# Kernel optimization log

Measured on AMD Instinct MI355X. Metric: run time of the kernel, lower is better.

## Reference

```python
import jax, jax.numpy as jnp
import numpy as np

NUM_HEADS = 16


def setup_inputs() -> dict:
    rng = jax.random.key(0)
    ks = jax.random.split(rng, 11)
    T, B, E = 1024, 4, 1024
    s = E ** -0.5  # weight init scale
    return {
        "query": jax.random.normal(ks[0], (T, B, E), jnp.float32),
        "key": jax.random.normal(ks[1], (T, B, E), jnp.float32),
        "value": jax.random.normal(ks[2], (T, B, E), jnp.float32),
        "q_proj_weight": jax.random.normal(ks[3], (E, E), jnp.float32) * s,
        "k_proj_weight1": jax.random.normal(ks[4], (E, E), jnp.float32) * s,
        "k_proj_weight2": jax.random.normal(ks[5], (E, E), jnp.float32) * s,
        "v_proj_weight": jax.random.normal(ks[6], (E, E), jnp.float32) * s,
        "in_proj_bias": jax.random.normal(ks[7], (4 * E,), jnp.float32) * 0.02,
        "out_proj_weight": jax.random.normal(ks[8], (E, E), jnp.float32) * s,
        "out_proj_bias": jax.random.normal(ks[9], (E,), jnp.float32) * 0.02,
        "pi": jax.random.uniform(ks[10], (2, NUM_HEADS), jnp.float32, 0.3, 0.7),
    }


def reference(query, key, value, q_proj_weight, k_proj_weight1, k_proj_weight2,
              v_proj_weight, in_proj_bias, out_proj_weight, out_proj_bias, pi):
    T, Bz, E = query.shape
    H = NUM_HEADS
    hd = E // H
    scaling = hd ** -0.5

    b_q, b_k1, b_k2, b_v = jnp.split(in_proj_bias, 4)
    q = query @ q_proj_weight.T + b_q
    k1 = key @ k_proj_weight1.T + b_k1
    k2 = key @ k_proj_weight2.T + b_k2
    v = value @ v_proj_weight.T + b_v

    def heads(x):  # (S, B, E) -> (B*H, S, hd)
        S = x.shape[0]
        return x.reshape(S, Bz * H, hd).transpose(1, 0, 2)

    q, k1, k2, v = heads(q), heads(k1), heads(k2), heads(v)

    def sqdist(a, b):  # (B*H, Nt, hd), (B*H, Ns, hd) -> (B*H, Nt, Ns)
        a2 = jnp.sum(a * a, axis=-1)
        b2 = jnp.sum(b * b, axis=-1)
        ab = jnp.einsum('btd,bsd->bts', a, b)
        return a2[:, :, None] + b2[:, None, :] - 2.0 * ab

    e1 = jnp.exp(-scaling / 2.0 * sqdist(q, k1))
    e2 = jnp.exp(-3.0 * scaling / 2.0 * sqdist(q, k2))

    pi1 = jnp.clip(jnp.abs(pi[0]), 1e-6, 2.0)  # (H,)
    pi2 = jnp.clip(jnp.abs(pi[1]), 1e-6, 2.0)

    Nt, Ns = e1.shape[1], e1.shape[2]
    attn = (e1.reshape(Bz, H, Nt, Ns) * pi1[None, :, None, None]
            + e2.reshape(Bz, H, Nt, Ns) * pi2[None, :, None, None])
    attn = attn.reshape(Bz * H, Nt, Ns)
    attn = attn / (jnp.sum(attn, axis=-1, keepdims=True) + 1e-6)

    out = jnp.einsum('bts,bsd->btd', attn, v)        # (B*H, Nt, hd)
    out = out.transpose(1, 0, 2).reshape(T, Bz, E)   # (T, B, E)
    return out @ out_proj_weight.T + out_proj_bias
```

## Files before the change

### kernel.cpp

```cpp
#include <hip/hip_runtime.h>
#include <hip/hip_bf16.h>

#define T_DIM 1024
#define B_DIM 4
#define E_DIM 1024
#define H_DIM 16
#define HD    64
#define M_DIM (T_DIM * B_DIM)

typedef __hip_bfloat16 bf16;
typedef __bf16 bf16x8 __attribute__((ext_vector_type(8)));
typedef __bf16 bf16x4 __attribute__((ext_vector_type(4)));
typedef float  f32x4  __attribute__((ext_vector_type(4)));

#define P4S ((size_t)M_DIM * E_DIM)
#define P1S ((size_t)E_DIM * E_DIM)

__global__ __launch_bounds__(256) void cvt_all(
    const float* __restrict__ q, const float* __restrict__ k,
    const float* __restrict__ v, const float* __restrict__ w0,
    const float* __restrict__ w1, const float* __restrict__ w2,
    const float* __restrict__ w3, const float* __restrict__ w4,
    __bf16* __restrict__ dst)
{
  size_t i = ((size_t)blockIdx.x * 256 + threadIdx.x) * 8;
  const float* src;
  size_t off;
  if (i < P4S)            { src = q; off = i; }
  else if (i < 2 * P4S)   { src = k; off = i - P4S; }
  else if (i < 3 * P4S)   { src = v; off = i - 2 * P4S; }
  else {
    size_t j = i - 3 * P4S;
    int wsel = (int)(j >> 20);
    off = j & (P1S - 1);
    const float* ws[5] = {w0, w1, w2, w3, w4};
    src = ws[wsel];
  }
  float4 a = *(const float4*)(src + off);
  float4 b = *(const float4*)(src + off + 4);
  bf16x8 o;
  o[0] = (__bf16)a.x; o[1] = (__bf16)a.y; o[2] = (__bf16)a.z; o[3] = (__bf16)a.w;
  o[4] = (__bf16)b.x; o[5] = (__bf16)b.y; o[6] = (__bf16)b.z; o[7] = (__bf16)b.w;
  *(bf16x8*)(dst + i) = o;
}

__device__ __forceinline__ void load_lds16(const __bf16* g, __bf16* l) {
  __builtin_amdgcn_global_load_lds(
      (__attribute__((address_space(1))) void*)(void*)g,
      (__attribute__((address_space(3))) void*)l, 16, 0, 0);
}
__device__ __forceinline__ void load_lds4(const float* g, float* l) {
  __builtin_amdgcn_global_load_lds(
      (__attribute__((address_space(1))) void*)(void*)g,
      (__attribute__((address_space(3))) void*)l, 4, 0, 0);
}

__device__ __forceinline__ void stage_half(
    int H, const __bf16* __restrict__ X, const __bf16* __restrict__ W,
    int bm, int bn, __bf16* As, __bf16* Bs, int tid)
{
  if (H >= 64) return;
  const int T  = H >> 2;
  const int h  = H & 3;
  const int rh = (h & 1) * 128;
  const __bf16* src = (h < 2) ? X : W;
  const int rbase   = (h < 2) ? bm : bn;
  __bf16* lb = ((h < 2) ? As : Bs) + (T & 1) * 16384;
#pragma unroll
  for (int li = 0; li < 2; ++li) {
    int r  = rh + li * 64 + (tid >> 3);
    int gc = (tid & 7) ^ (r & 7);
    load_lds16(src + (size_t)(rbase + r) * E_DIM + T * 64 + gc * 8,
               lb + (rh + li * 64) * 64 + tid * 8);
  }
}

#define RD(base, row, c) \
  (*(const bf16x8*)((base) + (row) * 64 + ((((c) ^ ((row) & 7))) << 3)))

__global__ __launch_bounds__(512, 2) void proj_gemm4(
    const __bf16* __restrict__ xbase, const __bf16* __restrict__ wbase,
    const float* __restrict__ bin, __bf16* __restrict__ cbase)
{
  __shared__ __bf16 lds[65536];
  __bf16* As = lds;
  __bf16* Bs = lds + 32768;

  const int z = blockIdx.z;
  const __bf16* X = xbase + ((z == 0) ? 0 : (z == 3) ? 2 * P4S : P4S);
  const __bf16* W = wbase + (size_t)z * P1S;
  const float* bias = bin + z * E_DIM;
  __bf16* C = cbase + (size_t)z * P4S;

  const int bm = blockIdx.x * 256;
  const int bn = blockIdx.y * 256;

  const int tid  = threadIdx.x;
  const int lane = tid & 63;
  const int w    = tid >> 6;
  const int wm   = w >> 2;
  const int wn   = w & 3;
  const int mrow = lane & 15, quad = lane >> 4;

  f32x4 acc[8][4];
#pragma unroll
  for (int m = 0; m < 8; ++m)
#pragma unroll
    for (int n = 0; n < 4; ++n) acc[m][n] = (f32x4)0.0f;

#pragma unroll
  for (int H = 0; H < 5; ++H) stage_half(H, X, W, bm, bn, As, Bs, tid);
  asm volatile("s_waitcnt vmcnt(2)" ::: "memory");
  __builtin_amdgcn_s_barrier();

  bf16x8 af[4][2];
  bf16x8 bq[4][2];

#pragma unroll 2
  for (int t = 0; t < 16; ++t) {
    const __bf16* Ab = As + (t & 1) * 16384;
    const __bf16* Bb = Bs + (t & 1) * 16384;

#pragma unroll
    for (int n = 0; n < 2; ++n)
#pragma unroll
      for (int kk = 0; kk < 2; ++kk)
        bq[n][kk] = RD(Bb, wn * 64 + n * 16 + mrow, kk * 4 + quad);
#pragma unroll
    for (int m = 0; m < 4; ++m)
#pragma unroll
      for (int kk = 0; kk < 2; ++kk)
        af[m][kk] = RD(Ab, wm * 128 + m * 16 + mrow, kk * 4 + quad);
    stage_half(4 * t + 5, X, W, bm, bn, As, Bs, tid);
    __builtin_amdgcn_s_barrier();
    asm volatile("s_waitcnt lgkmcnt(0)" ::: "memory");
    __builtin_amdgcn_s_setprio(1);
#pragma unroll
    for (int kk = 0; kk < 2; ++kk)
#pragma unroll
      for (int n = 0; n < 2; ++n)
#pragma unroll
        for (int m = 0; m < 4; ++m)
          acc[m][n] = __builtin_amdgcn_mfma_f32_16x16x32_bf16(
              af[m][kk], bq[n][kk], acc[m][n], 0, 0, 0);
    __builtin_amdgcn_s_setprio(0);
    __builtin_amdgcn_s_barrier();

#pragma unroll
    for (int n = 2; n < 4; ++n)
#pragma unroll
      for (int kk = 0; kk < 2; ++kk)
        bq[n][kk] = RD(Bb, wn * 64 + n * 16 + mrow, kk * 4 + quad);
    stage_half(4 * t + 6, X, W, bm, bn, As, Bs, tid);
    __builtin_amdgcn_s_barrier();
    asm volatile("s_waitcnt lgkmcnt(0)" ::: "memory");
    __builtin_amdgcn_s_setprio(1);
#pragma unroll
    for (int kk = 0; kk < 2; ++kk)
#pragma unroll
      for (int n = 2; n < 4; ++n)
#pragma unroll
        for (int m = 0; m < 4; ++m)
          acc[m][n] = __builtin_amdgcn_mfma_f32_16x16x32_bf16(
              af[m][kk], bq[n][kk], acc[m][n], 0, 0, 0);
    __builtin_amdgcn_s_setprio(0);
    __builtin_amdgcn_s_barrier();

#pragma unroll
    for (int m = 0; m < 4; ++m)
#pragma unroll
      for (int kk = 0; kk < 2; ++kk)
        af[m][kk] = RD(Ab, wm * 128 + 64 + m * 16 + mrow, kk * 4 + quad);
    stage_half(4 * t + 7, X, W, bm, bn, As, Bs, tid);
    __builtin_amdgcn_s_barrier();
    asm volatile("s_waitcnt lgkmcnt(0)" ::: "memory");
    __builtin_amdgcn_s_setprio(1);
#pragma unroll
    for (int kk = 0; kk < 2; ++kk)
#pragma unroll
      for (int n = 0; n < 2; ++n)
#pragma unroll
        for (int m = 0; m < 4; ++m)
          acc[4 + m][n] = __builtin_amdgcn_mfma_f32_16x16x32_bf16(
              af[m][kk], bq[n][kk], acc[4 + m][n], 0, 0, 0);
    __builtin_amdgcn_s_setprio(0);
    __builtin_amdgcn_s_barrier();

    stage_half(4 * t + 8, X, W, bm, bn, As, Bs, tid);
    __builtin_amdgcn_s_barrier();
    __builtin_amdgcn_s_setprio(1);
#pragma unroll
    for (int kk = 0; kk < 2; ++kk)
#pragma unroll
      for (int n = 2; n < 4; ++n)
#pragma unroll
        for (int m = 0; m < 4; ++m)
          acc[4 + m][n] = __builtin_amdgcn_mfma_f32_16x16x32_bf16(
              af[m][kk], bq[n][kk], acc[4 + m][n], 0, 0, 0);
    __builtin_amdgcn_s_setprio(0);
    if (t < 14)       { asm volatile("s_waitcnt vmcnt(2)" ::: "memory"); }
    else if (t == 14) { asm volatile("s_waitcnt vmcnt(0)" ::: "memory"); }
    __builtin_amdgcn_s_barrier();
  }

#pragma unroll
  for (int n = 0; n < 4; ++n) {
    int col = bn + wn * 64 + n * 16 + mrow;
    float bc = bias[col];
#pragma unroll
    for (int m = 0; m < 8; ++m) {
      int rbase = bm + wm * 128 + m * 16 + quad * 4;
#pragma unroll
      for (int r = 0; r < 4; ++r)
        C[(size_t)(rbase + r) * E_DIM + col] = (__bf16)(acc[m][n][r] + bc);
    }
  }
}

template <typename TO>
__device__ __forceinline__ void gemm_body(
    const __bf16* __restrict__ X, const __bf16* __restrict__ W,
    const float* __restrict__ bias, TO* __restrict__ C,
    int bm, int bn, int Ndim, int Kdim, __bf16* As, __bf16* Bs)
{
  const int tid  = threadIdx.x;
  const int lane = tid & 63;
  const int wave = tid >> 6;
  const int wy = (wave >> 1) * 64;
  const int wx = (wave & 1) * 64;
  const int mrow = lane & 15, quad = lane >> 4;

  const int srow = tid >> 2;
  const int ke   = (tid & 3) * 8;
  const __bf16* gA0 = X + (size_t)(bm + srow)      * Kdim + ke;
  const __bf16* gA1 = X + (size_t)(bm + srow + 64) * Kdim + ke;
  const __bf16* gB0 = W + (size_t)(bn + srow)      * Kdim + ke;
  const __bf16* gB1 = W + (size_t)(bn + srow + 64) * Kdim + ke;
  __bf16* lA0 = As + tid * 8;
  __bf16* lA1 = As + (tid + 256) * 8;
  __bf16* lB0 = Bs + tid * 8;
  __bf16* lB1 = Bs + (tid + 256) * 8;

  f32x4 acc[4][4];
#pragma unroll
  for (int i = 0; i < 4; ++i)
#pragma unroll
    for (int j = 0; j < 4; ++j) acc[i][j] = (f32x4)0.0f;

  for (int k0 = 0; k0 < Kdim; k0 += 32) {
    __syncthreads();
    load_lds16(gA0 + k0, lA0);
    load_lds16(gA1 + k0, lA1);
    load_lds16(gB0 + k0, lB0);
    load_lds16(gB1 + k0, lB1);
    __syncthreads();
    bf16x8 af[4], bf[4];
#pragma unroll
    for (int i = 0; i < 4; ++i)
      af[i] = *(const bf16x8*)(As + (wy + i * 16 + mrow) * 32 + quad * 8);
#pragma unroll
    for (int j = 0; j < 4; ++j)
      bf[j] = *(const bf16x8*)(Bs + (wx + j * 16 + mrow) * 32 + quad * 8);
#pragma unroll
    for (int i = 0; i < 4; ++i)
#pragma unroll
      for (int j = 0; j < 4; ++j)
        acc[i][j] = __builtin_amdgcn_mfma_f32_16x16x32_bf16(af[i], bf[j], acc[i][j], 0, 0, 0);
  }

#pragma unroll
  for (int j = 0; j < 4; ++j) {
    int col = bn + wx + j * 16 + mrow;
    float bc = bias[col];
#pragma unroll
    for (int i = 0; i < 4; ++i) {
      int rbase = bm + wy + i * 16 + quad * 4;
#pragma unroll
      for (int r = 0; r < 4; ++r)
        C[(size_t)(rbase + r) * Ndim + col] = (TO)(acc[i][j][r] + bc);
    }
  }
}

__global__ __launch_bounds__(256) void out_gemm(
    const __bf16* __restrict__ X, const __bf16* __restrict__ W,
    const float* __restrict__ bias, float* __restrict__ C)
{
  __shared__ __bf16 As[128 * 32];
  __shared__ __bf16 Bs[128 * 32];
  gemm_body<float>(X, W, bias, C, blockIdx.x * 128, blockIdx.y * 128,
                   E_DIM, E_DIM, As, Bs);
}

__global__ __launch_bounds__(256) void norms_vt(
    const __bf16* __restrict__ Qp, const __bf16* __restrict__ K1p,
    const __bf16* __restrict__ K2p, const __bf16* __restrict__ Vp,
    float* __restrict__ qn, float* __restrict__ kn1, float* __restrict__ kn2,
    __bf16* __restrict__ Vt_g)
{
  __shared__ __bf16 tile[64][88];
  const int tid = threadIdx.x;
  if (blockIdx.x < 768) {
    int id = blockIdx.x * 256 + tid;
    int which = id >> 16;
    int r = id & 65535;
    int bh = r >> 10, t = r & 1023;
    int b = bh >> 4, h = bh & 15;
    const __bf16* src = (which == 0) ? Qp : ((which == 1) ? K1p : K2p);
    float* dst = (which == 0) ? qn : ((which == 1) ? kn1 : kn2);
    const __bf16* p = src + (size_t)(t * 4 + b) * 1024 + h * 64;
    float s = 0.f;
#pragma unroll
    for (int c = 0; c < 8; ++c) {
      bf16x8 v = *(const bf16x8*)(p + c * 8);
#pragma unroll
      for (int j = 0; j < 8; ++j) { float x = (float)v[j]; s += x * x; }
    }
    dst[bh * 1024 + t] = s;
    return;
  }
  int bid = blockIdx.x - 768;
  const int bh = bid & 63, kt = bid >> 6;
  const int b = bh >> 4, h = bh & 15;
  {
    int s = tid >> 2, d0 = (tid & 3) * 16;
    const __bf16* src = Vp + (size_t)((kt * 64 + s) * 4 + b) * 1024 + h * 64 + d0;
    *(bf16x8*)(&tile[s][d0])     = *(const bf16x8*)(src);
    *(bf16x8*)(&tile[s][d0 + 8]) = *(const bf16x8*)(src + 8);
  }
  __syncthreads();
#pragma unroll
  for (int c = 0; c < 2; ++c) {
    int idx = tid * 2 + c;
    int d = idx >> 3, u0 = (idx & 7) * 8;
    bf16x8 o;
#pragma unroll
    for (int i = 0; i < 8; ++i) {
      int u = u0 + i;
      int s = (u & 3) * 16 + (u >> 2);
      o[i] = tile[s][d];
    }
    *(bf16x8*)(Vt_g + ((size_t)bh * 64 + d) * 1024 + kt * 64 + u0) = o;
  }
}

__global__ __launch_bounds__(256, 2) void mgk_attn_mfma(
    const __bf16* __restrict__ Qp, const __bf16* __restrict__ K1p,
    const __bf16* __restrict__ K2p, const __bf16* __restrict__ Vt_g,
    const float* __restrict__ qn_g, const float* __restrict__ kn1_g,
    const float* __restrict__ kn2_g, const float* __restrict__ pi,
    __bf16* __restrict__ AO)
{
  __shared__ __bf16 lds[36864];
  __bf16* Pl = lds + 24576;
  float* knl1 = (float*)(lds + 32768);
  float* knl2 = knl1 + 1024;

  const int bid = blockIdx.x;
  const int mm  = bid >> 3;
  const int bh  = (bid & 7) * 8 + (mm & 7);
  const int qt  = mm >> 3;
  const int b = bh >> 4, h = bh & 15;
  const int tid = threadIdx.x, lane = tid & 63, w = tid >> 6;
  const int mrow = lane & 15, quad = lane >> 4;

  const float cl1 = 0.0625f * 1.4426950408889634f;
  const float cl2 = 0.1875f * 1.4426950408889634f;
  const float L1 = 2.0f * cl1, L2 = 2.0f * cl2;
  const float p1 = fminf(fmaxf(fabsf(pi[h]), 1e-6f), 2.0f);
  const float p2 = fminf(fmaxf(fabsf(pi[H_DIM + h]), 1e-6f), 2.0f);
  const float lp1 = __log2f(p1), lp2 = __log2f(p2);
  const int hoff = h * 64;

  bf16x8 af[2][2];
  f32x4 aq2[2];
#pragma unroll
  for (int m = 0; m < 2; ++m) {
    const __bf16* qp = Qp + (size_t)((qt * 128 + w * 32 + m * 16 + mrow) * 4 + b) * 1024
                       + hoff + quad * 8;
    af[m][0] = *(const bf16x8*)(qp);
    af[m][1] = *(const bf16x8*)(qp + 32);
    f32x4 qnv = *(const f32x4*)(qn_g + bh * 1024 + qt * 128 + w * 32 + m * 16 + quad * 4);
#pragma unroll
    for (int r = 0; r < 4; ++r) aq2[m][r] = fmaf(cl1 - cl2, qnv[r], lp2);
  }

#pragma unroll
  for (int i = 0; i < 4; ++i) {
    load_lds4(kn1_g + bh * 1024 + i * 256 + tid, knl1 + i * 256 + tid);
    load_lds4(kn2_g + bh * 1024 + i * 256 + tid, knl2 + i * 256 + tid);
  }

#define STAGE_T(kt_, bsel_) do {                                              \
    __bf16* bb_ = lds + (bsel_) * 12288;                                      \
    _Pragma("unroll")                                                         \
    for (int li_ = 0; li_ < 2; ++li_) {                                       \
      int idx_ = li_ * 256 + tid;                                             \
      int row_ = idx_ >> 3;                                                   \
      int gc_  = (idx_ & 7) ^ (row_ & 7);                                     \
      size_t krow_ = (size_t)(((kt_) * 64 + row_) * 4 + b) * 1024 + hoff + gc_ * 8; \
      load_lds16(K1p + krow_, bb_ + idx_ * 8);                                \
      load_lds16(K2p + krow_, bb_ + 4096 + idx_ * 8);                         \
      load_lds16(Vt_g + ((size_t)bh * 64 + row_) * 1024 + (kt_) * 64 + gc_ * 8, \
                 bb_ + 8192 + idx_ * 8);                                      \
    }                                                                         \
  } while (0)

  STAGE_T(0, 0);
  STAGE_T(1, 1);
  asm volatile("s_waitcnt vmcnt(6)" ::: "memory");
  __builtin_amdgcn_s_barrier();

  f32x4 oacc[2][4];
#pragma unroll
  for (int m = 0; m < 2; ++m)
#pragma unroll
    for (int j = 0; j < 4; ++j) oacc[m][j] = (f32x4)0.0f;
  f32x4 rsl[2] = {(f32x4)0.0f, (f32x4)0.0f};

  for (int kt = 0; kt < 16; ++kt) {
    const int cur = kt & 1;
    const __bf16* K1s = lds + cur * 12288;
    const __bf16* K2s = K1s + 4096;
    const __bf16* Vt  = K1s + 8192;

    float f1[4], f2[4];
#pragma unroll
    for (int j = 0; j < 4; ++j) {
      f1[j] = knl1[kt * 64 + j * 16 + mrow];
      f2[j] = knl2[kt * 64 + j * 16 + mrow];
    }

    f32x4 acc1[2][4], acc2[2][4];
#pragma unroll
    for (int m = 0; m < 2; ++m)
#pragma unroll
      for (int j = 0; j < 4; ++j) { acc1[m][j] = (f32x4)0.0f; acc2[m][j] = (f32x4)0.0f; }
    __builtin_amdgcn_s_setprio(1);
#pragma unroll
    for (int kk = 0; kk < 2; ++kk)
#pragma unroll
      for (int j = 0; j < 4; ++j) {
        bf16x8 b1f = *(const bf16x8*)(K1s + (j * 16 + mrow) * 64
                                      + (((kk * 4 + quad) ^ (mrow & 7)) << 3));
        bf16x8 b2f = *(const bf16x8*)(K2s + (j * 16 + mrow) * 64
                                      + (((kk * 4 + quad) ^ (mrow & 7)) << 3));
#pragma unroll
        for (int m = 0; m < 2; ++m) {
          acc1[m][j] = __builtin_amdgcn_mfma_f32_16x16x32_bf16(af[m][kk], b1f, acc1[m][j], 0, 0, 0);
          acc2[m][j] = __builtin_amdgcn_mfma_f32_16x16x32_bf16(af[m][kk], b2f, acc2[m][j], 0, 0, 0);
        }
      }
    __builtin_amdgcn_s_setprio(0);

    float nb1[4], s2[4];
#pragma unroll
    for (int j = 0; j < 4; ++j) {
      nb1[j] = fmaf(-cl1, f1[j], lp1);
      s2[j]  = -cl2 * f2[j];
    }
#pragma unroll
    for (int m = 0; m < 2; ++m) {
      f32x4 pv[4];
#pragma unroll
      for (int j = 0; j < 4; ++j) {
        f32x4 p;
#pragma unroll
        for (int r = 0; r < 4; ++r) {
          float e1 = __builtin_amdgcn_exp2f(fmaf(L1, acc1[m][j][r], nb1[j]));
          float e2 = __builtin_amdgcn_exp2f(fmaf(L2, acc2[m][j][r], s2[j] + aq2[m][r]));
          p[r] = e1 + e2;
        }
        pv[j] = p;
        rsl[m] += p;
      }
#pragma unroll
      for (int r = 0; r < 4; ++r) {
        int q = m * 16 + quad * 4 + r;
        bf16x4 pk;
        pk[0] = (__bf16)pv[0][r]; pk[1] = (__bf16)pv[1][r];
        pk[2] = (__bf16)pv[2][r]; pk[3] = (__bf16)pv[3][r];
        int lc = mrow >> 1;
        *(bf16x4*)(Pl + w * 2048 + q * 64 + ((lc ^ (q & 7)) << 3) + (mrow & 1) * 4) = pk;
      }
    }

    bf16x8 pf[2][2];
#pragma unroll
    for (int m = 0; m < 2; ++m)
#pragma unroll
      for (int kk = 0; kk < 2; ++kk)
        pf[m][kk] = *(const bf16x8*)(Pl + w * 2048 + (m * 16 + mrow) * 64
                                     + (((kk * 4 + quad) ^ (mrow & 7)) << 3));
    __builtin_amdgcn_s_setprio(1);
#pragma unroll
    for (int kk = 0; kk < 2; ++kk)
#pragma unroll
      for (int j = 0; j < 4; ++j) {
        bf16x8 vf = *(const bf16x8*)(Vt + (j * 16 + mrow) * 64
                                     + (((kk * 4 + quad) ^ (mrow & 7)) << 3));
#pragma unroll
        for (int m = 0; m < 2; ++m)
          oacc[m][j] = __builtin_amdgcn_mfma_f32_16x16x32_bf16(pf[m][kk], vf, oacc[m][j], 0, 0, 0);
      }
    __builtin_amdgcn_s_setprio(0);

    if (kt < 15) {
      asm volatile("s_waitcnt lgkmcnt(0)" ::: "memory");
      __builtin_amdgcn_s_barrier();
      if (kt < 14) {
        STAGE_T(kt + 2, cur);
        asm volatile("s_waitcnt vmcnt(6)" ::: "memory");
      } else {
        asm volatile("s_waitcnt vmcnt(0)" ::: "memory");
      }
      __builtin_amdgcn_s_barrier();
      asm volatile("" ::: "memory");
    }
  }
#undef STAGE_T

#pragma unroll
  for (int m = 0; m < 2; ++m) {
#pragma unroll
    for (int d = 1; d < 16; d <<= 1) {
      f32x4 o;
#pragma unroll
      for (int r = 0; r < 4; ++r) o[r] = __shfl_xor(rsl[m][r], d, 64);
      rsl[m] += o;
    }
    f32x4 inv;
#pragma unroll
    for (int r = 0; r < 4; ++r) inv[r] = 1.0f / (rsl[m][r] + 1e-6f);
#pragma unroll
    for (int j = 0; j < 4; ++j) {
      int col = hoff + j * 16 + mrow;
#pragma unroll
      for (int r = 0; r < 4; ++r) {
        int t = qt * 128 + w * 32 + m * 16 + quad * 4 + r;
        AO[(size_t)(t * 4 + b) * 1024 + col] = (__bf16)(oacc[m][j][r] * inv[r]);
      }
    }
  }
}

extern "C" void kernel_launch(void* const* d_in, const int* in_sizes, int n_in,
                              void* d_out, int out_size, void* d_ws, size_t ws_size,
                              hipStream_t stream) {
  const float* query = (const float*)d_in[0];
  const float* key   = (const float*)d_in[1];
  const float* value = (const float*)d_in[2];
  const float* Wq    = (const float*)d_in[3];
  const float* Wk1   = (const float*)d_in[4];
  const float* Wk2   = (const float*)d_in[5];
  const float* Wv    = (const float*)d_in[6];
  const float* bin   = (const float*)d_in[7];
  const float* Wo    = (const float*)d_in[8];
  const float* bo    = (const float*)d_in[9];
  const float* pi    = (const float*)d_in[10];
  float* out = (float*)d_out;

  __bf16* qc  = (__bf16*)d_ws;
  __bf16* wq  = qc  + 3 * P4S;
  __bf16* wo  = wq  + 4 * P1S;
  __bf16* Qp  = wq  + 5 * P1S;
  __bf16* K1p = Qp  + P4S;
  __bf16* K2p = K1p + P4S;
  __bf16* Vp  = K2p + P4S;
  __bf16* AO  = Vp  + P4S;
  float*  qn_g  = (float*)(AO + P4S);
  float*  kn1_g = qn_g  + 64 * 1024;
  float*  kn2_g = kn1_g + 64 * 1024;
  __bf16* Vt_g  = qc;

  cvt_all<<<8704, 256, 0, stream>>>(query, key, value, Wq, Wk1, Wk2, Wv, Wo, qc);

  proj_gemm4<<<dim3(M_DIM / 256, E_DIM / 256, 4), 512, 0, stream>>>(qc, wq, bin, Qp);

  norms_vt<<<768 + 1024, 256, 0, stream>>>(Qp, K1p, K2p, Vp,
                                           qn_g, kn1_g, kn2_g, Vt_g);

  mgk_attn_mfma<<<512, 256, 0, stream>>>(
      Qp, K1p, K2p, Vt_g, qn_g, kn1_g, kn2_g, pi, AO);

  out_gemm<<<dim3(M_DIM / 128, E_DIM / 128), 256, 0, stream>>>(AO, wo, bo, out);
}
```

Measured before the change: 239.5 us.

## Fuse row norms into projection GEMM and split attention keys across wave groups

The squared row norms of Q, K1 and K2 are now computed in the projection GEMM epilogue from the rounded bf16 outputs, so the separate norm pass over the projected tensors goes away and K norms are written in an interleaved layout. The attention kernel moves to 512 threads with two wave groups. Each group processes half of the key tiles in 32-key steps with its own double buffer, and the partial outputs and row sums are combined through LDS at the end. The aim is more parallelism per block and less launch and memory traffic, at the cost of an extra LDS reduction, more barriers and a reshuffled V-transpose layout.

```diff
diff --git a/kernel.cpp b/kernel.cpp
--- a/kernel.cpp
+++ b/kernel.cpp
@@ -11,6 +11,7 @@
 typedef __hip_bfloat16 bf16;
 typedef __bf16 bf16x8 __attribute__((ext_vector_type(8)));
 typedef __bf16 bf16x4 __attribute__((ext_vector_type(4)));
+typedef __bf16 bf16x2 __attribute__((ext_vector_type(2)));
 typedef float  f32x4  __attribute__((ext_vector_type(4)));
 
 #define P4S ((size_t)M_DIM * E_DIM)
@@ -49,11 +50,6 @@
       (__attribute__((address_space(1))) void*)(void*)g,
       (__attribute__((address_space(3))) void*)l, 16, 0, 0);
 }
-__device__ __forceinline__ void load_lds4(const float* g, float* l) {
-  __builtin_amdgcn_global_load_lds(
-      (__attribute__((address_space(1))) void*)(void*)g,
-      (__attribute__((address_space(3))) void*)l, 4, 0, 0);
-}
 
 __device__ __forceinline__ void stage_half(
     int H, const __bf16* __restrict__ X, const __bf16* __restrict__ W,
@@ -80,7 +76,8 @@
 
 __global__ __launch_bounds__(512, 2) void proj_gemm4(
     const __bf16* __restrict__ xbase, const __bf16* __restrict__ wbase,
-    const float* __restrict__ bin, __bf16* __restrict__ cbase)
+    const float* __restrict__ bin, __bf16* __restrict__ cbase,
+    float* __restrict__ qn_g, float* __restrict__ knr_g)
 {
   __shared__ __bf16 lds[65536];
   __bf16* As = lds;
@@ -203,6 +200,9 @@
     __builtin_amdgcn_s_barrier();
   }
 
+  f32x4 ns[8];
+#pragma unroll
+  for (int m = 0; m < 8; ++m) ns[m] = (f32x4)0.0f;
 #pragma unroll
   for (int n = 0; n < 4; ++n) {
     int col = bn + wn * 64 + n * 16 + mrow;
@@ -211,8 +211,40 @@
     for (int m = 0; m < 8; ++m) {
       int rbase = bm + wm * 128 + m * 16 + quad * 4;
 #pragma unroll
-      for (int r = 0; r < 4; ++r)
-        C[(size_t)(rbase + r) * E_DIM + col] = (__bf16)(acc[m][n][r] + bc);
+      for (int r = 0; r < 4; ++r) {
+        __bf16 xb = (__bf16)(acc[m][n][r] + bc);
+        C[(size_t)(rbase + r) * E_DIM + col] = xb;
+        float xv = (float)xb;
+        ns[m][r] = fmaf(xv, xv, ns[m][r]);
+      }
+    }
+  }
+  if (z < 3) {
+#pragma unroll
+    for (int m = 0; m < 8; ++m)
+#pragma unroll
+      for (int d = 1; d < 16; d <<= 1) {
+        f32x4 o;
+#pragma unroll
+        for (int r = 0; r < 4; ++r) o[r] = __shfl_xor(ns[m][r], d, 64);
+        ns[m] += o;
+      }
+    if (mrow == 0) {
+      int hh = (bn >> 6) + wn;
+#pragma unroll
+      for (int m = 0; m < 8; ++m) {
+        int t = (bm >> 2) + wm * 32 + m * 4 + quad;
+#pragma unroll
+        for (int r = 0; r < 4; ++r) {
+          int bhh = r * 16 + hh;
+          float v = ns[m][r];
+          if (z == 0)
+            qn_g[bhh * 1024 + t] = v;
+          else
+            knr_g[bhh * 2048 + (t >> 5) * 64 + ((z == 2) ? 32 : 0)
+                  + (t & 15) * 2 + ((t >> 4) & 1)] = v;
+        }
+      }
     }
   }
 }
@@ -292,35 +324,12 @@
                    E_DIM, E_DIM, As, Bs);
 }
 
-__global__ __launch_bounds__(256) void norms_vt(
-    const __bf16* __restrict__ Qp, const __bf16* __restrict__ K1p,
-    const __bf16* __restrict__ K2p, const __bf16* __restrict__ Vp,
-    float* __restrict__ qn, float* __restrict__ kn1, float* __restrict__ kn2,
-    __bf16* __restrict__ Vt_g)
+__global__ __launch_bounds__(256) void vt_only(
+    const __bf16* __restrict__ Vp, __bf16* __restrict__ Vt_g)
 {
   __shared__ __bf16 tile[64][88];
   const int tid = threadIdx.x;
-  if (blockIdx.x < 768) {
-    int id = blockIdx.x * 256 + tid;
-    int which = id >> 16;
-    int r = id & 65535;
-    int bh = r >> 10, t = r & 1023;
-    int b = bh >> 4, h = bh & 15;
-    const __bf16* src = (which == 0) ? Qp : ((which == 1) ? K1p : K2p);
-    float* dst = (which == 0) ? qn : ((which == 1) ? kn1 : kn2);
-    const __bf16* p = src + (size_t)(t * 4 + b) * 1024 + h * 64;
-    float s = 0.f;
-#pragma unroll
-    for (int c = 0; c < 8; ++c) {
-      bf16x8 v = *(const bf16x8*)(p + c * 8);
-#pragma unroll
-      for (int j = 0; j < 8; ++j) { float x = (float)v[j]; s += x * x; }
-    }
-    dst[bh * 1024 + t] = s;
-    return;
-  }
-  int bid = blockIdx.x - 768;
-  const int bh = bid & 63, kt = bid >> 6;
+  const int bh = blockIdx.x & 63, kt = blockIdx.x >> 6;
   const int b = bh >> 4, h = bh & 15;
   {
     int s = tid >> 2, d0 = (tid & 3) * 16;
@@ -337,31 +346,29 @@
 #pragma unroll
     for (int i = 0; i < 8; ++i) {
       int u = u0 + i;
-      int s = (u & 3) * 16 + (u >> 2);
+      int s = (u >> 5) * 32 + ((u & 31) >> 1) + (u & 1) * 16;
       o[i] = tile[s][d];
     }
     *(bf16x8*)(Vt_g + ((size_t)bh * 64 + d) * 1024 + kt * 64 + u0) = o;
   }
 }
 
-__global__ __launch_bounds__(256, 2) void mgk_attn_mfma(
+__global__ __launch_bounds__(512, 4) void mgk_attn_mfma(
     const __bf16* __restrict__ Qp, const __bf16* __restrict__ K1p,
     const __bf16* __restrict__ K2p, const __bf16* __restrict__ Vt_g,
-    const float* __restrict__ qn_g, const float* __restrict__ kn1_g,
-    const float* __restrict__ kn2_g, const float* __restrict__ pi,
-    __bf16* __restrict__ AO)
+    const float* __restrict__ qn_g, const float* __restrict__ knr_g,
+    const float* __restrict__ pi, __bf16* __restrict__ AO)
 {
-  __shared__ __bf16 lds[36864];
-  __bf16* Pl = lds + 24576;
-  float* knl1 = (float*)(lds + 32768);
-  float* knl2 = knl1 + 1024;
+  __shared__ __bf16 lds[33280];
+  __bf16* Pl = lds + 25088;
 
   const int bid = blockIdx.x;
-  const int mm  = bid >> 3;
-  const int bh  = (bid & 7) * 8 + (mm & 7);
-  const int qt  = mm >> 3;
+  const int bh  = (bid & 7) * 8 + ((bid >> 3) & 7);
+  const int qt  = bid >> 6;
   const int b = bh >> 4, h = bh & 15;
   const int tid = threadIdx.x, lane = tid & 63, w = tid >> 6;
+  const int g = w >> 2, wg = w & 3;
+  const int gtid = tid & 255;
   const int mrow = lane & 15, quad = lane >> 4;
 
   const float cl1 = 0.0625f * 1.4426950408889634f;
@@ -376,39 +383,35 @@
   f32x4 aq2[2];
 #pragma unroll
   for (int m = 0; m < 2; ++m) {
-    const __bf16* qp = Qp + (size_t)((qt * 128 + w * 32 + m * 16 + mrow) * 4 + b) * 1024
+    const __bf16* qp = Qp + (size_t)((qt * 128 + wg * 32 + m * 16 + mrow) * 4 + b) * 1024
                        + hoff + quad * 8;
     af[m][0] = *(const bf16x8*)(qp);
     af[m][1] = *(const bf16x8*)(qp + 32);
-    f32x4 qnv = *(const f32x4*)(qn_g + bh * 1024 + qt * 128 + w * 32 + m * 16 + quad * 4);
+    f32x4 qnv = *(const f32x4*)(qn_g + bh * 1024 + qt * 128 + wg * 32 + m * 16 + quad * 4);
 #pragma unroll
     for (int r = 0; r < 4; ++r) aq2[m][r] = fmaf(cl1 - cl2, qnv[r], lp2);
   }
 
-#pragma unroll
-  for (int i = 0; i < 4; ++i) {
-    load_lds4(kn1_g + bh * 1024 + i * 256 + tid, knl1 + i * 256 + tid);
-    load_lds4(kn2_g + bh * 1024 + i * 256 + tid, knl2 + i * 256 + tid);
-  }
-
-#define STAGE_T(kt_, bsel_) do {                                              \
-    __bf16* bb_ = lds + (bsel_) * 12288;                                      \
-    _Pragma("unroll")                                                         \
-    for (int li_ = 0; li_ < 2; ++li_) {                                       \
-      int idx_ = li_ * 256 + tid;                                             \
-      int row_ = idx_ >> 3;                                                   \
-      int gc_  = (idx_ & 7) ^ (row_ & 7);                                     \
-      size_t krow_ = (size_t)(((kt_) * 64 + row_) * 4 + b) * 1024 + hoff + gc_ * 8; \
-      load_lds16(K1p + krow_, bb_ + idx_ * 8);                                \
-      load_lds16(K2p + krow_, bb_ + 4096 + idx_ * 8);                         \
-      load_lds16(Vt_g + ((size_t)bh * 64 + row_) * 1024 + (kt_) * 64 + gc_ * 8, \
-                 bb_ + 8192 + idx_ * 8);                                      \
-    }                                                                         \
+  const int srK = gtid >> 3;
+  const int gcK = (gtid & 7) ^ (srK & 7);
+  const __bf16* gK1 = K1p + (size_t)(srK * 4 + b) * 1024 + hoff + gcK * 8;
+  const __bf16* gVt = Vt_g + ((size_t)bh * 64 + (gtid >> 2)) * 1024 + (gtid & 3) * 8;
+  const float*  gkn = knr_g + bh * 2048 + wg * 16 + lane * 4;
+
+#define STAGE_T(i_, bsel_) do {                                               \
+    __bf16* bb_ = lds + (bsel_) * 6272;                                       \
+    int kt_ = g * 16 + (i_);                                                  \
+    load_lds16(gK1 + (size_t)kt_ * 131072,       bb_ + gtid * 8);             \
+    load_lds16(gK1 + P4S + (size_t)kt_ * 131072, bb_ + 2048 + gtid * 8);      \
+    load_lds16(gVt + kt_ * 32,                   bb_ + 4096 + gtid * 8);      \
+    if (lane < 4)                                                             \
+      load_lds16((const __bf16*)(gkn + kt_ * 64),                             \
+                 bb_ + 6144 + wg * 32 + lane * 8);                            \
   } while (0)
 
-  STAGE_T(0, 0);
-  STAGE_T(1, 1);
-  asm volatile("s_waitcnt vmcnt(6)" ::: "memory");
+  STAGE_T(0, g * 2);
+  STAGE_T(1, g * 2 + 1);
+  asm volatile("s_waitcnt vmcnt(4)" ::: "memory");
   __builtin_amdgcn_s_barrier();
 
   f32x4 oacc[2][4];
@@ -418,33 +421,33 @@
     for (int j = 0; j < 4; ++j) oacc[m][j] = (f32x4)0.0f;
   f32x4 rsl[2] = {(f32x4)0.0f, (f32x4)0.0f};
 
-  for (int kt = 0; kt < 16; ++kt) {
-    const int cur = kt & 1;
-    const __bf16* K1s = lds + cur * 12288;
-    const __bf16* K2s = K1s + 4096;
-    const __bf16* Vt  = K1s + 8192;
-
-    float f1[4], f2[4];
-#pragma unroll
-    for (int j = 0; j < 4; ++j) {
-      f1[j] = knl1[kt * 64 + j * 16 + mrow];
-      f2[j] = knl2[kt * 64 + j * 16 + mrow];
-    }
-
-    f32x4 acc1[2][4], acc2[2][4];
+  for (int i = 0; i < 16; ++i) {
+    __bf16* buf = lds + (g * 2 + (i & 1)) * 6272;
+    const __bf16* K1s = buf;
+    const __bf16* K2s = buf + 2048;
+    const __bf16* Vts = buf + 4096;
+    const float*  knb = (const float*)(buf + 6144);
+
+    float2 f1 = *(const float2*)(knb + mrow * 2);
+    float2 f2 = *(const float2*)(knb + 32 + mrow * 2);
+    float nb1[2], s2v[2];
+    nb1[0] = fmaf(-cl1, f1.x, lp1); nb1[1] = fmaf(-cl1, f1.y, lp1);
+    s2v[0] = -cl2 * f2.x;           s2v[1] = -cl2 * f2.y;
+
+    f32x4 acc1[2][2], acc2[2][2];
 #pragma unroll
     for (int m = 0; m < 2; ++m)
 #pragma unroll
-      for (int j = 0; j < 4; ++j) { acc1[m][j] = (f32x4)0.0f; acc2[m][j] = (f32x4)0.0f; }
+      for (int j = 0; j < 2; ++j) { acc1[m][j] = (f32x4)0.0f; acc2[m][j] = (f32x4)0.0f; }
     __builtin_amdgcn_s_setprio(1);
 #pragma unroll
     for (int kk = 0; kk < 2; ++kk)
 #pragma unroll
-      for (int j = 0; j < 4; ++j) {
-        bf16x8 b1f = *(const bf16x8*)(K1s + (j * 16 + mrow) * 64
-                                      + (((kk * 4 + quad) ^ (mrow & 7)) << 3));
-        bf16x8 b2f = *(const bf16x8*)(K2s + (j * 16 + mrow) * 64
-                                      + (((kk * 4 + quad) ^ (mrow & 7)) << 3));
+      for (int j = 0; j < 2; ++j) {
+        int row = j * 16 + mrow;
+        int off = row * 64 + (((kk * 4 + quad) ^ (row & 7)) << 3);
+        bf16x8 b1f = *(const bf16x8*)(K1s + off);
+        bf16x8 b2f = *(const bf16x8*)(K2s + off);
 #pragma unroll
         for (int m = 0; m < 2; ++m) {
           acc1[m][j] = __builtin_amdgcn_mfma_f32_16x16x32_bf16(af[m][kk], b1f, acc1[m][j], 0, 0, 0);
@@ -453,92 +456,106 @@
       }
     __builtin_amdgcn_s_setprio(0);
 
-    float nb1[4], s2[4];
-#pragma unroll
-    for (int j = 0; j < 4; ++j) {
-      nb1[j] = fmaf(-cl1, f1[j], lp1);
-      s2[j]  = -cl2 * f2[j];
-    }
 #pragma unroll
     for (int m = 0; m < 2; ++m) {
-      f32x4 pv[4];
-#pragma unroll
-      for (int j = 0; j < 4; ++j) {
+      f32x4 pj[2];
+#pragma unroll
+      for (int j = 0; j < 2; ++j) {
         f32x4 p;
 #pragma unroll
         for (int r = 0; r < 4; ++r) {
           float e1 = __builtin_amdgcn_exp2f(fmaf(L1, acc1[m][j][r], nb1[j]));
-          float e2 = __builtin_amdgcn_exp2f(fmaf(L2, acc2[m][j][r], s2[j] + aq2[m][r]));
+          float e2 = __builtin_amdgcn_exp2f(fmaf(L2, acc2[m][j][r], s2v[j] + aq2[m][r]));
           p[r] = e1 + e2;
         }
-        pv[j] = p;
+        pj[j] = p;
         rsl[m] += p;
       }
 #pragma unroll
       for (int r = 0; r < 4; ++r) {
         int q = m * 16 + quad * 4 + r;
-        bf16x4 pk;
-        pk[0] = (__bf16)pv[0][r]; pk[1] = (__bf16)pv[1][r];
-        pk[2] = (__bf16)pv[2][r]; pk[3] = (__bf16)pv[3][r];
-        int lc = mrow >> 1;
-        *(bf16x4*)(Pl + w * 2048 + q * 64 + ((lc ^ (q & 7)) << 3) + (mrow & 1) * 4) = pk;
-      }
-    }
-
-    bf16x8 pf[2][2];
+        bf16x2 pk; pk[0] = (__bf16)pj[0][r]; pk[1] = (__bf16)pj[1][r];
+        *(bf16x2*)(Pl + w * 1024 + q * 32 + mrow * 2) = pk;
+      }
+    }
+
+    bf16x8 pf[2];
 #pragma unroll
     for (int m = 0; m < 2; ++m)
-#pragma unroll
-      for (int kk = 0; kk < 2; ++kk)
-        pf[m][kk] = *(const bf16x8*)(Pl + w * 2048 + (m * 16 + mrow) * 64
-                                     + (((kk * 4 + quad) ^ (mrow & 7)) << 3));
+      pf[m] = *(const bf16x8*)(Pl + w * 1024 + (m * 16 + mrow) * 32 + quad * 8);
     __builtin_amdgcn_s_setprio(1);
 #pragma unroll
-    for (int kk = 0; kk < 2; ++kk)
-#pragma unroll
-      for (int j = 0; j < 4; ++j) {
-        bf16x8 vf = *(const bf16x8*)(Vt + (j * 16 + mrow) * 64
-                                     + (((kk * 4 + quad) ^ (mrow & 7)) << 3));
-#pragma unroll
-        for (int m = 0; m < 2; ++m)
-          oacc[m][j] = __builtin_amdgcn_mfma_f32_16x16x32_bf16(pf[m][kk], vf, oacc[m][j], 0, 0, 0);
-      }
+    for (int j = 0; j < 4; ++j) {
+      bf16x8 vf = *(const bf16x8*)(Vts + (j * 16 + mrow) * 32 + quad * 8);
+#pragma unroll
+      for (int m = 0; m < 2; ++m)
+        oacc[m][j] = __builtin_amdgcn_mfma_f32_16x16x32_bf16(pf[m], vf, oacc[m][j], 0, 0, 0);
+    }
     __builtin_amdgcn_s_setprio(0);
 
-    if (kt < 15) {
+    if (i < 15) {
       asm volatile("s_waitcnt lgkmcnt(0)" ::: "memory");
       __builtin_amdgcn_s_barrier();
-      if (kt < 14) {
-        STAGE_T(kt + 2, cur);
-        asm volatile("s_waitcnt vmcnt(6)" ::: "memory");
+      if (i < 14) {
+        STAGE_T(i + 2, g * 2 + (i & 1));
+        asm volatile("s_waitcnt vmcnt(4)" ::: "memory");
       } else {
         asm volatile("s_waitcnt vmcnt(0)" ::: "memory");
       }
       __builtin_amdgcn_s_barrier();
-      asm volatile("" ::: "memory");
     }
   }
 #undef STAGE_T
 
-#pragma unroll
-  for (int m = 0; m < 2; ++m) {
-#pragma unroll
-    for (int d = 1; d < 16; d <<= 1) {
-      f32x4 o;
-#pragma unroll
-      for (int r = 0; r < 4; ++r) o[r] = __shfl_xor(rsl[m][r], d, 64);
-      rsl[m] += o;
-    }
-    f32x4 inv;
-#pragma unroll
-    for (int r = 0; r < 4; ++r) inv[r] = 1.0f / (rsl[m][r] + 1e-6f);
-#pragma unroll
-    for (int j = 0; j < 4; ++j) {
-      int col = hoff + j * 16 + mrow;
-#pragma unroll
-      for (int r = 0; r < 4; ++r) {
-        int t = qt * 128 + w * 32 + m * 16 + quad * 4 + r;
-        AO[(size_t)(t * 4 + b) * 1024 + col] = (__bf16)(oacc[m][j][r] * inv[r]);
+  __builtin_amdgcn_s_barrier();
+  float* Of = (float*)lds;
+  float* Rf = (float*)Pl;
+  if (g == 1) {
+#pragma unroll
+    for (int m = 0; m < 2; ++m) {
+#pragma unroll
+      for (int j = 0; j < 4; ++j)
+#pragma unroll
+        for (int r = 0; r < 4; ++r)
+          Of[(wg * 32 + m * 16 + quad * 4 + r) * 64 + j * 16 + mrow] = oacc[m][j][r];
+#pragma unroll
+      for (int r = 0; r < 4; ++r)
+        Rf[(wg * 32 + m * 16 + quad * 4 + r) * 16 + mrow] = rsl[m][r];
+    }
+  }
+  __builtin_amdgcn_s_barrier();
+  if (g == 0) {
+#pragma unroll
+    for (int m = 0; m < 2; ++m) {
+#pragma unroll
+      for (int j = 0; j < 4; ++j)
+#pragma unroll
+        for (int r = 0; r < 4; ++r)
+          oacc[m][j][r] += Of[(wg * 32 + m * 16 + quad * 4 + r) * 64 + j * 16 + mrow];
+#pragma unroll
+      for (int r = 0; r < 4; ++r)
+        rsl[m][r] += Rf[(wg * 32 + m * 16 + quad * 4 + r) * 16 + mrow];
+    }
+#pragma unroll
+    for (int m = 0; m < 2; ++m) {
+#pragma unroll
+      for (int d = 1; d < 16; d <<= 1) {
+        f32x4 o;
+#pragma unroll
+        for (int r = 0; r < 4; ++r) o[r] = __shfl_xor(rsl[m][r], d, 64);
+        rsl[m] += o;
+      }
+      f32x4 inv;
+#pragma unroll
+      for (int r = 0; r < 4; ++r) inv[r] = 1.0f / (rsl[m][r] + 1e-6f);
+#pragma unroll
+      for (int j = 0; j < 4; ++j) {
+        int col = hoff + j * 16 + mrow;
+#pragma unroll
+        for (int r = 0; r < 4; ++r) {
+          int t = qt * 128 + wg * 32 + m * 16 + quad * 4 + r;
+          AO[(size_t)(t * 4 + b) * 1024 + col] = (__bf16)(oacc[m][j][r] * inv[r]);
+        }
       }
     }
   }
@@ -568,20 +585,19 @@
   __bf16* K2p = K1p + P4S;
   __bf16* Vp  = K2p + P4S;
   __bf16* AO  = Vp  + P4S;
-  float*  qn_g  = (float*)(AO + P4S);
-  float*  kn1_g = qn_g  + 64 * 1024;
-  float*  kn2_g = kn1_g + 64 * 1024;
-  __bf16* Vt_g  = qc;
+  float*  qn_g = (float*)(AO + P4S);
+  float*  knr  = qn_g + 64 * 1024;
+  __bf16* Vt_g = qc;
 
   cvt_all<<<8704, 256, 0, stream>>>(query, key, value, Wq, Wk1, Wk2, Wv, Wo, qc);
 
-  proj_gemm4<<<dim3(M_DIM / 256, E_DIM / 256, 4), 512, 0, stream>>>(qc, wq, bin, Qp);
-
-  norms_vt<<<768 + 1024, 256, 0, stream>>>(Qp, K1p, K2p, Vp,
-                                           qn_g, kn1_g, kn2_g, Vt_g);
-
-  mgk_attn_mfma<<<512, 256, 0, stream>>>(
-      Qp, K1p, K2p, Vt_g, qn_g, kn1_g, kn2_g, pi, AO);
+  proj_gemm4<<<dim3(M_DIM / 256, E_DIM / 256, 4), 512, 0, stream>>>(
+      qc, wq, bin, Qp, qn_g, knr);
+
+  vt_only<<<1024, 256, 0, stream>>>(Vp, Vt_g);
+
+  mgk_attn_mfma<<<512, 512, 0, stream>>>(
+      Qp, K1p, K2p, Vt_g, qn_g, knr, pi, AO);
 
   out_gemm<<<dim3(M_DIM / 128, E_DIM / 128), 256, 0, stream>>>(AO, wo, bo, out);
 }
```

Result: slower. 264.3 us (+10.4%).
